# Kernel optimization log

Hardware: AMD Instinct MI355X
Metric: run time of the kernel (lower is better)

## Reference

```python
import jax, jax.numpy as jnp
import numpy as np

N_HEAD = 12
SEQ = 4096
D_MODEL = 768


def setup_inputs() -> dict:
    key = jax.random.key(0)
    ks = jax.random.split(key, 5)
    tokens = jax.random.normal(ks[0], (SEQ, D_MODEL), dtype=jnp.float32)
    # GPT-2 causal mask buffer: lower-triangular ones, shape [1,1,n_ctx,n_ctx]
    attn_bias = jnp.tril(jnp.ones((SEQ, SEQ), dtype=jnp.float32))[None, None]
    c_attn_weight = jax.random.normal(ks[1], (D_MODEL, 3 * D_MODEL), dtype=jnp.float32) * 0.02
    c_attn_bias = jax.random.normal(ks[2], (3 * D_MODEL,), dtype=jnp.float32) * 0.02
    c_proj_weight = jax.random.normal(ks[3], (D_MODEL, D_MODEL), dtype=jnp.float32) * 0.02
    c_proj_bias = jax.random.normal(ks[4], (D_MODEL,), dtype=jnp.float32) * 0.02
    return {
        "tokens": tokens,
        "attn_bias": attn_bias,
        "c_attn_weight": c_attn_weight,
        "c_attn_bias": c_attn_bias,
        "c_proj_weight": c_proj_weight,
        "c_proj_bias": c_proj_bias,
    }


def reference(tokens, attn_bias, c_attn_weight, c_attn_bias, c_proj_weight, c_proj_bias):
    S, D = tokens.shape
    H = N_HEAD
    hd = D // H
    qkv = tokens @ c_attn_weight + c_attn_bias          # [S, 3D]
    q, k, v = jnp.split(qkv, 3, axis=1)                 # each [S, D]
    q = q.reshape(S, H, hd).transpose(1, 0, 2)          # [H, S, hd]
    kh = k.reshape(S, H, hd).transpose(1, 2, 0)         # [H, hd, S] (key pre-transposed)
    vh = v.reshape(S, H, hd).transpose(1, 0, 2)         # [H, S, hd]
    w = jnp.einsum('hqd,hdk->hqk', q, kh) / jnp.sqrt(jnp.float32(hd))  # [H, S, S]
    nd, ns = S, S
    b = attn_bias[0, :, ns - nd:ns, :ns]                # [1, S, S], broadcasts over heads
    w = w * b - 1e10 * (1.0 - b)
    p = jax.nn.softmax(w, axis=-1)
    a = jnp.einsum('hqk,hkd->hqd', p, vh)               # [H, S, hd]
    a = a.transpose(1, 0, 2).reshape(S, D)              # merge heads
    out = a @ c_proj_weight + c_proj_bias               # [S, D]
    return out
```

## Files before the change

### kernel.cpp

```cpp
#include <hip/hip_runtime.h>

typedef __attribute__((ext_vector_type(8))) short s8v;
typedef __attribute__((ext_vector_type(4))) float f32x4;
typedef __attribute__((ext_vector_type(4))) unsigned short u16x4;
typedef __attribute__((ext_vector_type(2))) unsigned int u32x2;

#define SEQ 4096
#define DM  768
#define NH  12
#define HD  64

__device__ __forceinline__ unsigned short f2bf(float f) {
  union { float f; unsigned int u; } v; v.f = f;
  unsigned int r = v.u + 0x7fffu + ((v.u >> 16) & 1u);
  return (unsigned short)(r >> 16);
}

__device__ __forceinline__ unsigned int cvtpk(float lo, float hi) {
  unsigned int r;
  asm("v_cvt_pk_bf16_f32 %0, %1, %2" : "=v"(r) : "v"(lo), "v"(hi));
  return r;
}

__device__ __forceinline__ void gload16(const void* g, void* l) {
  __builtin_amdgcn_global_load_lds((const __attribute__((address_space(1))) void*)g,
                                   (__attribute__((address_space(3))) void*)l, 16, 0, 0);
}

__global__ __launch_bounds__(256) void k_cast(const float* __restrict__ in,
                                              unsigned short* __restrict__ out) {
  int i = (blockIdx.x * 256 + threadIdx.x) * 4;
  float4 v = *reinterpret_cast<const float4*>(in + i);
  u16x4 o;
  o.x = f2bf(v.x); o.y = f2bf(v.y); o.z = f2bf(v.z); o.w = f2bf(v.w);
  *reinterpret_cast<u16x4*>(out + i) = o;
}

__global__ __launch_bounds__(256) void k_transpose_cast(const float* __restrict__ in,
                                                        unsigned short* __restrict__ out,
                                                        int K, int N) {
  __shared__ float tile[32][33];
  int k0 = blockIdx.x * 32, n0 = blockIdx.y * 32;
  int tr = threadIdx.x >> 5, tc = threadIdx.x & 31;
#pragma unroll
  for (int i = 0; i < 4; i++)
    tile[i * 8 + tr][tc] = in[(k0 + i * 8 + tr) * N + n0 + tc];
  __syncthreads();
#pragma unroll
  for (int i = 0; i < 4; i++)
    out[(n0 + i * 8 + tr) * K + k0 + tc] = f2bf(tile[tc][i * 8 + tr]);
}

template<int MODE>
__global__ __launch_bounds__(256) void k_gemm(
    const unsigned short* __restrict__ A, const unsigned short* __restrict__ BT,
    const float* __restrict__ bias,
    unsigned short* __restrict__ Oq, unsigned short* __restrict__ Ok,
    unsigned short* __restrict__ Ov, float* __restrict__ Of) {
  __shared__ unsigned short As[128 * 32];
  __shared__ unsigned short Bs[128 * 32];
  const int tid = threadIdx.x;
  const int lane = tid & 63;
  const int w = tid >> 6;
  const int wm = w >> 1, wn = w & 1;
  const int l15 = lane & 15, l4 = lane >> 4;
  const int m0 = blockIdx.x * 128, n0 = blockIdx.y * 128;

  f32x4 acc[4][4] = {};

  int srow[2], skc[2];
#pragma unroll
  for (int j = 0; j < 2; j++) {
    int slot = j * 256 + tid;
    srow[j] = slot >> 2;
    skc[j] = (slot & 3) ^ ((srow[j] >> 1) & 3);
  }
  const int ldsb0 = (tid & ~63) * 16;
  const int ldsb1 = (256 + (tid & ~63)) * 16;

  for (int k0 = 0; k0 < DM; k0 += 32) {
    gload16(A + (m0 + srow[0]) * DM + k0 + skc[0] * 8, (char*)As + ldsb0);
    gload16(A + (m0 + srow[1]) * DM + k0 + skc[1] * 8, (char*)As + ldsb1);
    gload16(BT + (n0 + srow[0]) * DM + k0 + skc[0] * 8, (char*)Bs + ldsb0);
    gload16(BT + (n0 + srow[1]) * DM + k0 + skc[1] * 8, (char*)Bs + ldsb1);
    __syncthreads();
    s8v af[4], bfr[4];
#pragma unroll
    for (int i = 0; i < 4; i++) {
      int ra = wm * 64 + i * 16 + l15;
      int ca = (l4 ^ ((ra >> 1) & 3)) * 8;
      af[i] = *reinterpret_cast<const s8v*>(&As[ra * 32 + ca]);
      int rb = wn * 64 + i * 16 + l15;
      int cb = (l4 ^ ((rb >> 1) & 3)) * 8;
      bfr[i] = *reinterpret_cast<const s8v*>(&Bs[rb * 32 + cb]);
    }
#pragma unroll
    for (int mi = 0; mi < 4; mi++)
#pragma unroll
      for (int nj = 0; nj < 4; nj++)
        acc[mi][nj] = __builtin_amdgcn_mfma_f32_16x16x32_bf16(af[mi], bfr[nj], acc[mi][nj], 0, 0, 0);
    __syncthreads();
  }

#pragma unroll
  for (int nj = 0; nj < 4; nj++) {
    const int col = n0 + wn * 64 + nj * 16 + l15;
    const float bv = bias[col];
#pragma unroll
    for (int mi = 0; mi < 4; mi++) {
      const int rowb = m0 + wm * 64 + mi * 16 + l4 * 4;
      if (MODE == 0) {
        if (col < 768) {
#pragma unroll
          for (int r = 0; r < 4; r++)
            Oq[(rowb + r) * DM + col] = f2bf(acc[mi][nj][r] + bv);
        } else if (col < 1536) {
#pragma unroll
          for (int r = 0; r < 4; r++)
            Ok[(rowb + r) * DM + (col - 768)] = f2bf(acc[mi][nj][r] + bv);
        } else {
          u16x4 pk;
#pragma unroll
          for (int r = 0; r < 4; r++)
            pk[r] = f2bf(acc[mi][nj][r] + bv);
          *reinterpret_cast<u16x4*>(&Ov[(col - 1536) * SEQ + rowb]) = pk;
        }
      } else {
#pragma unroll
        for (int r = 0; r < 4; r++)
          Of[(rowb + r) * DM + col] = acc[mi][nj][r] + bv;
      }
    }
  }
}

__global__ __launch_bounds__(256, 4) void k_attn(
    const unsigned short* __restrict__ Qb, const unsigned short* __restrict__ Kb,
    const unsigned short* __restrict__ Vt, float* __restrict__ Opart,
    float* __restrict__ mlw) {
  __shared__ unsigned short Ks[2][64 * 64];
  __shared__ unsigned short Vs[2][64 * 64];
  __shared__ unsigned char Pl[4][2048];
  const int tid = threadIdx.x;
  const int lane = tid & 63;
  const int w = tid >> 6;
  const int l15 = lane & 15, l4 = lane >> 4;
  const int bid = blockIdx.x;
  const int s = bid & 1;
  const int b2 = bid >> 1;
  const int h = b2 % NH;
  const int qt = 63 - (b2 / NH);
  const int q0 = qt * 64 + w * 16;
  const int ntiles = qt + 1;
  const float SCL = 0.125f * 1.44269504f;

  const unsigned short* const Kh = Kb + h * HD;
  const unsigned short* const Vh = Vt + h * HD * SEQ;

  int srow[2], scol[2];
#pragma unroll
  for (int j = 0; j < 2; j++) {
    int c = j * 256 + tid;
    srow[j] = c >> 3;
    scol[j] = ((c & 7) ^ (srow[j] & 7)) * 8;
  }
  const int ldsoff0 = (tid & ~63) * 16;
  const int ldsoff1 = 4096 + (tid & ~63) * 16;

  s8v aq[2];
#pragma unroll
  for (int kc = 0; kc < 2; kc++)
    aq[kc] = *reinterpret_cast<const s8v*>(&Qb[(q0 + l15) * DM + h * HD + kc * 32 + l4 * 8]);

  const int kvbase = l15 * 128 + ((l4 ^ (l15 & 7)) << 4);

  unsigned char* const pw = (unsigned char*)&Pl[w][0];
  const int swz = (l15 & 7) << 4;
  const int wr_base = l15 * 128 + l4 * 8;
  const int rd_base = l15 * 128 + l4 * 16;
  const int lanediff = l15 - l4 * 4;

  f32x4 Ot[4] = {};
  float m = -1e30f, lsum = 0.f;

  if (s < ntiles) {
    const int kb0 = s * 64;
    gload16(Kh + (kb0 + srow[0]) * DM + scol[0], (char*)Ks[0] + ldsoff0);
    gload16(Kh + (kb0 + srow[1]) * DM + scol[1], (char*)Ks[0] + ldsoff1);
    gload16(Vh + srow[0] * SEQ + kb0 + scol[0], (char*)Vs[0] + ldsoff0);
    gload16(Vh + srow[1] * SEQ + kb0 + scol[1], (char*)Vs[0] + ldsoff1);
    __asm__ volatile("s_waitcnt vmcnt(0)" ::: "memory");
  }
  __syncthreads();

  for (int t = s; t < ntiles; t += 2) {
    const int cur = ((t - s) >> 1) & 1;
    if (t + 2 < ntiles) {
      const int kb2 = (t + 2) * 64;
      const int nxt = cur ^ 1;
      gload16(Kh + (kb2 + srow[0]) * DM + scol[0], (char*)Ks[nxt] + ldsoff0);
      gload16(Kh + (kb2 + srow[1]) * DM + scol[1], (char*)Ks[nxt] + ldsoff1);
      gload16(Vh + srow[0] * SEQ + kb2 + scol[0], (char*)Vs[nxt] + ldsoff0);
      gload16(Vh + srow[1] * SEQ + kb2 + scol[1], (char*)Vs[nxt] + ldsoff1);
    }
    const int kb = t * 64;
    const char* const kbuf = (const char*)Ks[cur];
    const char* const vbuf = (const char*)Vs[cur];

    float p[4][4];
#pragma unroll
    for (int c2 = 0; c2 < 4; c2++) {
      const s8v k0 = *reinterpret_cast<const s8v*>(kbuf + (c2 * 2048 + kvbase));
      const s8v k1 = *reinterpret_cast<const s8v*>(kbuf + ((c2 * 2048 + kvbase) ^ 64));
      f32x4 z = {};
      z = __builtin_amdgcn_mfma_f32_16x16x32_bf16(k0, aq[0], z, 0, 0, 0);
      z = __builtin_amdgcn_mfma_f32_16x16x32_bf16(k1, aq[1], z, 0, 0, 0);
#pragma unroll
      for (int r = 0; r < 4; r++) p[c2][r] = z[r];
    }
    if (kb + 63 > q0) {
      const int qml = q0 - kb + lanediff;
#pragma unroll
      for (int c2 = 0; c2 < 4; c2++)
#pragma unroll
        for (int r = 0; r < 4; r++)
          p[c2][r] = (c2 * 16 + r > qml) ? -1e30f : p[c2][r];
    }
    float t0 = fmaxf(fmaxf(p[0][0], p[0][1]), fmaxf(p[0][2], p[0][3]));
    float t1 = fmaxf(fmaxf(p[1][0], p[1][1]), fmaxf(p[1][2], p[1][3]));
    float t2 = fmaxf(fmaxf(p[2][0], p[2][1]), fmaxf(p[2][2], p[2][3]));
    float t3 = fmaxf(fmaxf(p[3][0], p[3][1]), fmaxf(p[3][2], p[3][3]));
    float tm = fmaxf(fmaxf(t0, t1), fmaxf(t2, t3));
    tm = fmaxf(tm, __shfl_xor(tm, 16));
    tm = fmaxf(tm, __shfl_xor(tm, 32));
    const float tsc = tm * SCL;
    if (!__all(tsc <= m + 8.f)) {
      const float mn = fmaxf(m, tsc);
      const float al = exp2f(m - mn);
      m = mn;
      lsum *= al;
#pragma unroll
      for (int dc = 0; dc < 4; dc++)
#pragma unroll
        for (int r = 0; r < 4; r++) Ot[dc][r] *= al;
    }
    float sacc = 0.f;
#pragma unroll
    for (int c2 = 0; c2 < 4; c2++) {
      float e0 = exp2f(fmaf(p[c2][0], SCL, -m));
      float e1 = exp2f(fmaf(p[c2][1], SCL, -m));
      float e2 = exp2f(fmaf(p[c2][2], SCL, -m));
      float e3 = exp2f(fmaf(p[c2][3], SCL, -m));
      sacc += (e0 + e1) + (e2 + e3);
      u32x2 pk;
      pk.x = cvtpk(e0, e1);
      pk.y = cvtpk(e2, e3);
      *reinterpret_cast<u32x2*>(pw + ((wr_base + c2 * 32) ^ swz)) = pk;
    }
    lsum += sacc;
    __asm__ volatile("s_waitcnt lgkmcnt(0)" ::: "memory");
    const s8v pb0 = *reinterpret_cast<const s8v*>(pw + (rd_base ^ swz));
    const s8v pb1 = *reinterpret_cast<const s8v*>(pw + ((rd_base + 64) ^ swz));
#pragma unroll
    for (int dc = 0; dc < 4; dc++) {
      const s8v v0 = *reinterpret_cast<const s8v*>(vbuf + (dc * 2048 + kvbase));
      const s8v v1 = *reinterpret_cast<const s8v*>(vbuf + ((dc * 2048 + kvbase) ^ 64));
      Ot[dc] = __builtin_amdgcn_mfma_f32_16x16x32_bf16(v0, pb0, Ot[dc], 0, 0, 0);
      Ot[dc] = __builtin_amdgcn_mfma_f32_16x16x32_bf16(v1, pb1, Ot[dc], 0, 0, 0);
    }
    __asm__ volatile("s_waitcnt vmcnt(0)" ::: "memory");
    __syncthreads();
  }

  lsum += __shfl_xor(lsum, 16);
  lsum += __shfl_xor(lsum, 32);
  float* const op = Opart + (size_t)s * SEQ * DM + (q0 + l15) * DM + h * HD;
#pragma unroll
  for (int dc = 0; dc < 4; dc++)
    *reinterpret_cast<f32x4*>(op + dc * 16 + l4 * 4) = Ot[dc];
  if (l4 == 0) {
    float2* const mp = (float2*)mlw;
    mp[(s * NH + h) * SEQ + q0 + l15] = make_float2(m, lsum);
  }
}

__global__ __launch_bounds__(256) void k_merge(const float* __restrict__ Opart,
                                               const float* __restrict__ mlw,
                                               unsigned short* __restrict__ attn) {
  const int idx = blockIdx.x * 256 + threadIdx.x;
  const int e4 = idx * 4;
  const int row = e4 / DM;
  const int col = e4 - row * DM;
  const int h = col >> 6;
  const float2* mp = (const float2*)mlw;
  const float2 a = mp[h * SEQ + row];
  const float2 b = mp[(NH + h) * SEQ + row];
  const float ms = fmaxf(a.x, b.x);
  const float w0 = exp2f(a.x - ms), w1 = exp2f(b.x - ms);
  const float rl = 1.f / (w0 * a.y + w1 * b.y);
  const float4 o0 = *reinterpret_cast<const float4*>(Opart + e4);
  const float4 o1 = *reinterpret_cast<const float4*>(Opart + (size_t)SEQ * DM + e4);
  u16x4 pk;
  pk.x = f2bf((w0 * o0.x + w1 * o1.x) * rl);
  pk.y = f2bf((w0 * o0.y + w1 * o1.y) * rl);
  pk.z = f2bf((w0 * o0.z + w1 * o1.z) * rl);
  pk.w = f2bf((w0 * o0.w + w1 * o1.w) * rl);
  *reinterpret_cast<u16x4*>(attn + e4) = pk;
}

extern "C" void kernel_launch(void* const* d_in, const int* in_sizes, int n_in,
                              void* d_out, int out_size, void* d_ws, size_t ws_size,
                              hipStream_t stream) {
  (void)in_sizes; (void)n_in; (void)out_size; (void)ws_size;
  const float* tokens = (const float*)d_in[0];
  const float* wqkv  = (const float*)d_in[2];
  const float* bqkv  = (const float*)d_in[3];
  const float* wproj = (const float*)d_in[4];
  const float* bproj = (const float*)d_in[5];
  float* out = (float*)d_out;

  unsigned short* tok    = (unsigned short*)d_ws;
  unsigned short* wqkvT  = tok + 4096 * 768;
  unsigned short* wprojT = wqkvT + 2304 * 768;
  unsigned short* Qb     = wprojT + 768 * 768;
  unsigned short* Kb     = Qb + 4096 * 768;
  unsigned short* Vt     = Kb + 4096 * 768;
  unsigned short* attn   = Vt + 768 * 4096;
  float* Opart = (float*)(attn + 4096 * 768);
  float* mlw   = Opart + 2 * 4096 * 768;

  k_cast<<<3072, 256, 0, stream>>>(tokens, tok);
  k_transpose_cast<<<dim3(24, 72), 256, 0, stream>>>(wqkv, wqkvT, 768, 2304);
  k_transpose_cast<<<dim3(24, 24), 256, 0, stream>>>(wproj, wprojT, 768, 768);
  k_gemm<0><<<dim3(32, 18), 256, 0, stream>>>(tok, wqkvT, bqkv, Qb, Kb, Vt, nullptr);
  k_attn<<<1536, 256, 0, stream>>>(Qb, Kb, Vt, Opart, mlw);
  k_merge<<<3072, 256, 0, stream>>>(Opart, mlw, attn);
  k_gemm<1><<<dim3(32, 6), 256, 0, stream>>>(attn, wprojT, bproj, nullptr, nullptr, nullptr, out);
}
```

Measured before the change: 119.1 us.

## Rework attention to 32x32 MFMA tiles with register-resident P and 4-way KV split

The attention kernel now uses 32x32x16 bf16 MFMAs with 128-query blocks (32 rows per wave). The softmax probabilities are repacked in registers via permlane32 swaps instead of going through an LDS round trip. The softmax scale and log2e are folded into Q inside the QKV GEMM epilogue. KV tiles are split across 4 blocks instead of 2, and the merge kernel combines four partials. This cuts LDS traffic and per-tile softmax instructions, but doubles the partial-output memory traffic in the merge and adds causal-skip imbalance.

New measurement: 138.1 us. 1.16x slower.

```diff
diff --git a/kernel.cpp b/kernel.cpp
--- a/kernel.cpp
+++ b/kernel.cpp
@@ -2,13 +2,15 @@
 
 typedef __attribute__((ext_vector_type(8))) short s8v;
 typedef __attribute__((ext_vector_type(4))) float f32x4;
+typedef __attribute__((ext_vector_type(16))) float f32x16;
 typedef __attribute__((ext_vector_type(4))) unsigned short u16x4;
-typedef __attribute__((ext_vector_type(2))) unsigned int u32x2;
+typedef __attribute__((ext_vector_type(4))) unsigned int u32x4;
 
 #define SEQ 4096
 #define DM  768
 #define NH  12
 #define HD  64
+#define QSCL 0.18033688f
 
 __device__ __forceinline__ unsigned short f2bf(float f) {
   union { float f; unsigned int u; } v; v.f = f;
@@ -113,7 +115,7 @@
         if (col < 768) {
 #pragma unroll
           for (int r = 0; r < 4; r++)
-            Oq[(rowb + r) * DM + col] = f2bf(acc[mi][nj][r] + bv);
+            Oq[(rowb + r) * DM + col] = f2bf((acc[mi][nj][r] + bv) * QSCL);
         } else if (col < 1536) {
 #pragma unroll
           for (int r = 0; r < 4; r++)
@@ -134,28 +136,26 @@
   }
 }
 
-__global__ __launch_bounds__(256, 4) void k_attn(
+__global__ __launch_bounds__(256, 5) void k_attn(
     const unsigned short* __restrict__ Qb, const unsigned short* __restrict__ Kb,
     const unsigned short* __restrict__ Vt, float* __restrict__ Opart,
     float* __restrict__ mlw) {
   __shared__ unsigned short Ks[2][64 * 64];
   __shared__ unsigned short Vs[2][64 * 64];
-  __shared__ unsigned char Pl[4][2048];
   const int tid = threadIdx.x;
   const int lane = tid & 63;
   const int w = tid >> 6;
-  const int l15 = lane & 15, l4 = lane >> 4;
+  const int l31 = lane & 31, lh = lane >> 5;
   const int bid = blockIdx.x;
-  const int s = bid & 1;
-  const int b2 = bid >> 1;
-  const int h = b2 % NH;
-  const int qt = 63 - (b2 / NH);
-  const int q0 = qt * 64 + w * 16;
-  const int ntiles = qt + 1;
-  const float SCL = 0.125f * 1.44269504f;
-
-  const unsigned short* const Kh = Kb + h * HD;
-  const unsigned short* const Vh = Vt + h * HD * SEQ;
+  const int s = bid & 3;
+  const int b2 = bid >> 2;
+  const int head = b2 % NH;
+  const int qt = 31 - (b2 / NH);
+  const int q0w = qt * 128 + w * 32;
+  const int ntiles = 2 * qt + 2;
+
+  const unsigned short* const Kh = Kb + head * HD;
+  const unsigned short* const Vh = Vt + head * HD * SEQ;
 
   int srow[2], scol[2];
 #pragma unroll
@@ -167,20 +167,16 @@
   const int ldsoff0 = (tid & ~63) * 16;
   const int ldsoff1 = 4096 + (tid & ~63) * 16;
 
-  s8v aq[2];
-#pragma unroll
-  for (int kc = 0; kc < 2; kc++)
-    aq[kc] = *reinterpret_cast<const s8v*>(&Qb[(q0 + l15) * DM + h * HD + kc * 32 + l4 * 8]);
-
-  const int kvbase = l15 * 128 + ((l4 ^ (l15 & 7)) << 4);
-
-  unsigned char* const pw = (unsigned char*)&Pl[w][0];
-  const int swz = (l15 & 7) << 4;
-  const int wr_base = l15 * 128 + l4 * 8;
-  const int rd_base = l15 * 128 + l4 * 16;
-  const int lanediff = l15 - l4 * 4;
-
-  f32x4 Ot[4] = {};
+  s8v aq[4];
+#pragma unroll
+  for (int kc = 0; kc < 4; kc++)
+    aq[kc] = *reinterpret_cast<const s8v*>(
+        &Qb[(q0w + l31) * DM + head * HD + kc * 16 + lh * 8]);
+
+  const int x7 = l31 & 7;
+  const int rbase = l31 * 128;
+
+  f32x16 O0 = {}, O1 = {};
   float m = -1e30f, lsum = 0.f;
 
   if (s < ntiles) {
@@ -193,10 +189,10 @@
   }
   __syncthreads();
 
-  for (int t = s; t < ntiles; t += 2) {
-    const int cur = ((t - s) >> 1) & 1;
-    if (t + 2 < ntiles) {
-      const int kb2 = (t + 2) * 64;
+  for (int t = s; t < ntiles; t += 4) {
+    const int cur = ((t - s) >> 2) & 1;
+    if (t + 4 < ntiles) {
+      const int kb2 = (t + 4) * 64;
       const int nxt = cur ^ 1;
       gload16(Kh + (kb2 + srow[0]) * DM + scol[0], (char*)Ks[nxt] + ldsoff0);
       gload16(Kh + (kb2 + srow[1]) * DM + scol[1], (char*)Ks[nxt] + ldsoff1);
@@ -204,83 +200,94 @@
       gload16(Vh + srow[1] * SEQ + kb2 + scol[1], (char*)Vs[nxt] + ldsoff1);
     }
     const int kb = t * 64;
-    const char* const kbuf = (const char*)Ks[cur];
-    const char* const vbuf = (const char*)Vs[cur];
-
-    float p[4][4];
-#pragma unroll
-    for (int c2 = 0; c2 < 4; c2++) {
-      const s8v k0 = *reinterpret_cast<const s8v*>(kbuf + (c2 * 2048 + kvbase));
-      const s8v k1 = *reinterpret_cast<const s8v*>(kbuf + ((c2 * 2048 + kvbase) ^ 64));
-      f32x4 z = {};
-      z = __builtin_amdgcn_mfma_f32_16x16x32_bf16(k0, aq[0], z, 0, 0, 0);
-      z = __builtin_amdgcn_mfma_f32_16x16x32_bf16(k1, aq[1], z, 0, 0, 0);
-#pragma unroll
-      for (int r = 0; r < 4; r++) p[c2][r] = z[r];
-    }
-    if (kb + 63 > q0) {
-      const int qml = q0 - kb + lanediff;
-#pragma unroll
-      for (int c2 = 0; c2 < 4; c2++)
-#pragma unroll
-        for (int r = 0; r < 4; r++)
-          p[c2][r] = (c2 * 16 + r > qml) ? -1e30f : p[c2][r];
-    }
-    float t0 = fmaxf(fmaxf(p[0][0], p[0][1]), fmaxf(p[0][2], p[0][3]));
-    float t1 = fmaxf(fmaxf(p[1][0], p[1][1]), fmaxf(p[1][2], p[1][3]));
-    float t2 = fmaxf(fmaxf(p[2][0], p[2][1]), fmaxf(p[2][2], p[2][3]));
-    float t3 = fmaxf(fmaxf(p[3][0], p[3][1]), fmaxf(p[3][2], p[3][3]));
-    float tm = fmaxf(fmaxf(t0, t1), fmaxf(t2, t3));
-    tm = fmaxf(tm, __shfl_xor(tm, 16));
-    tm = fmaxf(tm, __shfl_xor(tm, 32));
-    const float tsc = tm * SCL;
-    if (!__all(tsc <= m + 8.f)) {
-      const float mn = fmaxf(m, tsc);
-      const float al = exp2f(m - mn);
-      m = mn;
-      lsum *= al;
-#pragma unroll
-      for (int dc = 0; dc < 4; dc++)
-#pragma unroll
-        for (int r = 0; r < 4; r++) Ot[dc][r] *= al;
-    }
-    float sacc = 0.f;
-#pragma unroll
-    for (int c2 = 0; c2 < 4; c2++) {
-      float e0 = exp2f(fmaf(p[c2][0], SCL, -m));
-      float e1 = exp2f(fmaf(p[c2][1], SCL, -m));
-      float e2 = exp2f(fmaf(p[c2][2], SCL, -m));
-      float e3 = exp2f(fmaf(p[c2][3], SCL, -m));
-      sacc += (e0 + e1) + (e2 + e3);
-      u32x2 pk;
-      pk.x = cvtpk(e0, e1);
-      pk.y = cvtpk(e2, e3);
-      *reinterpret_cast<u32x2*>(pw + ((wr_base + c2 * 32) ^ swz)) = pk;
-    }
-    lsum += sacc;
-    __asm__ volatile("s_waitcnt lgkmcnt(0)" ::: "memory");
-    const s8v pb0 = *reinterpret_cast<const s8v*>(pw + (rd_base ^ swz));
-    const s8v pb1 = *reinterpret_cast<const s8v*>(pw + ((rd_base + 64) ^ swz));
-#pragma unroll
-    for (int dc = 0; dc < 4; dc++) {
-      const s8v v0 = *reinterpret_cast<const s8v*>(vbuf + (dc * 2048 + kvbase));
-      const s8v v1 = *reinterpret_cast<const s8v*>(vbuf + ((dc * 2048 + kvbase) ^ 64));
-      Ot[dc] = __builtin_amdgcn_mfma_f32_16x16x32_bf16(v0, pb0, Ot[dc], 0, 0, 0);
-      Ot[dc] = __builtin_amdgcn_mfma_f32_16x16x32_bf16(v1, pb1, Ot[dc], 0, 0, 0);
+    if (kb <= q0w + 31) {
+      const char* const kbuf = (const char*)Ks[cur];
+      const char* const vbuf = (const char*)Vs[cur];
+      f32x16 z0 = {}, z1 = {};
+#pragma unroll
+      for (int kc = 0; kc < 4; kc++) {
+        const int so = ((kc * 2 + lh) ^ x7) << 4;
+        const s8v k0 = *reinterpret_cast<const s8v*>(kbuf + rbase + so);
+        const s8v k1 = *reinterpret_cast<const s8v*>(kbuf + 4096 + rbase + so);
+        z0 = __builtin_amdgcn_mfma_f32_32x32x16_bf16(k0, aq[kc], z0, 0, 0, 0);
+        z1 = __builtin_amdgcn_mfma_f32_32x32x16_bf16(k1, aq[kc], z1, 0, 0, 0);
+      }
+      float p0[16], p1[16];
+#pragma unroll
+      for (int r = 0; r < 16; r++) { p0[r] = z0[r]; p1[r] = z1[r]; }
+      if (kb + 63 > q0w) {
+        const int qm = q0w + l31 - kb - 4 * lh;
+#pragma unroll
+        for (int r = 0; r < 16; r++) {
+          const int koff = (r & 3) + 8 * (r >> 2);
+          p0[r] = (koff > qm) ? -1e30f : p0[r];
+          p1[r] = (koff + 32 > qm) ? -1e30f : p1[r];
+        }
+      }
+      float tm = p0[0];
+#pragma unroll
+      for (int r = 1; r < 16; r++) tm = fmaxf(tm, p0[r]);
+#pragma unroll
+      for (int r = 0; r < 16; r++) tm = fmaxf(tm, p1[r]);
+      tm = fmaxf(tm, __shfl_xor(tm, 32));
+      if (!__all(tm <= m + 8.f)) {
+        const float mn = fmaxf(m, tm);
+        const float al = exp2f(m - mn);
+        m = mn;
+        lsum *= al;
+#pragma unroll
+        for (int r = 0; r < 16; r++) { O0[r] *= al; O1[r] *= al; }
+      }
+      float sacc = 0.f;
+#pragma unroll
+      for (int r = 0; r < 16; r++) { p0[r] = exp2f(p0[r] - m); sacc += p0[r]; }
+#pragma unroll
+      for (int r = 0; r < 16; r++) { p1[r] = exp2f(p1[r] - m); sacc += p1[r]; }
+      lsum += sacc;
+      s8v pf[4];
+#define PACKKC(pp, dst)                                                      \
+      {                                                                      \
+        unsigned int A0 = cvtpk(pp[0], pp[1]);                               \
+        unsigned int B0 = cvtpk(pp[2], pp[3]);                               \
+        unsigned int A1 = cvtpk(pp[4], pp[5]);                               \
+        unsigned int B1 = cvtpk(pp[6], pp[7]);                               \
+        asm("v_permlane32_swap_b32 %0, %1" : "+v"(A0), "+v"(A1));            \
+        asm("v_permlane32_swap_b32 %0, %1" : "+v"(B0), "+v"(B1));            \
+        u32x4 q_ = {A0, B0, A1, B1};                                         \
+        dst = __builtin_bit_cast(s8v, q_);                                   \
+      }
+      PACKKC(p0, pf[0]);
+      PACKKC((p0 + 8), pf[1]);
+      PACKKC(p1, pf[2]);
+      PACKKC((p1 + 8), pf[3]);
+#undef PACKKC
+#pragma unroll
+      for (int kc = 0; kc < 4; kc++) {
+        const int so = ((kc * 2 + lh) ^ x7) << 4;
+        const s8v v0 = *reinterpret_cast<const s8v*>(vbuf + rbase + so);
+        const s8v v1 = *reinterpret_cast<const s8v*>(vbuf + 4096 + rbase + so);
+        O0 = __builtin_amdgcn_mfma_f32_32x32x16_bf16(v0, pf[kc], O0, 0, 0, 0);
+        O1 = __builtin_amdgcn_mfma_f32_32x32x16_bf16(v1, pf[kc], O1, 0, 0, 0);
+      }
     }
     __asm__ volatile("s_waitcnt vmcnt(0)" ::: "memory");
     __syncthreads();
   }
 
-  lsum += __shfl_xor(lsum, 16);
   lsum += __shfl_xor(lsum, 32);
-  float* const op = Opart + (size_t)s * SEQ * DM + (q0 + l15) * DM + h * HD;
-#pragma unroll
-  for (int dc = 0; dc < 4; dc++)
-    *reinterpret_cast<f32x4*>(op + dc * 16 + l4 * 4) = Ot[dc];
-  if (l4 == 0) {
+  float* const op = Opart + (size_t)s * SEQ * DM + (size_t)(q0w + l31) * DM +
+                    head * HD + 4 * lh;
+#pragma unroll
+  for (int k = 0; k < 4; k++) {
+    f32x4 o0, o1;
+#pragma unroll
+    for (int r = 0; r < 4; r++) { o0[r] = O0[k * 4 + r]; o1[r] = O1[k * 4 + r]; }
+    *reinterpret_cast<f32x4*>(op + 8 * k) = o0;
+    *reinterpret_cast<f32x4*>(op + 32 + 8 * k) = o1;
+  }
+  if (lh == 0) {
     float2* const mp = (float2*)mlw;
-    mp[(s * NH + h) * SEQ + q0 + l15] = make_float2(m, lsum);
+    mp[(s * NH + head) * SEQ + q0w + l31] = make_float2(m, lsum);
   }
 }
 
@@ -291,20 +298,26 @@
   const int e4 = idx * 4;
   const int row = e4 / DM;
   const int col = e4 - row * DM;
-  const int h = col >> 6;
+  const int head = col >> 6;
   const float2* mp = (const float2*)mlw;
-  const float2 a = mp[h * SEQ + row];
-  const float2 b = mp[(NH + h) * SEQ + row];
-  const float ms = fmaxf(a.x, b.x);
-  const float w0 = exp2f(a.x - ms), w1 = exp2f(b.x - ms);
-  const float rl = 1.f / (w0 * a.y + w1 * b.y);
+  const float2 a0 = mp[(0 * NH + head) * SEQ + row];
+  const float2 a1 = mp[(1 * NH + head) * SEQ + row];
+  const float2 a2 = mp[(2 * NH + head) * SEQ + row];
+  const float2 a3 = mp[(3 * NH + head) * SEQ + row];
+  const float ms = fmaxf(fmaxf(a0.x, a1.x), fmaxf(a2.x, a3.x));
+  const float w0 = exp2f(a0.x - ms), w1 = exp2f(a1.x - ms);
+  const float w2 = exp2f(a2.x - ms), w3 = exp2f(a3.x - ms);
+  const float rl = 1.f / (w0 * a0.y + w1 * a1.y + w2 * a2.y + w3 * a3.y);
+  const size_t SD = (size_t)SEQ * DM;
   const float4 o0 = *reinterpret_cast<const float4*>(Opart + e4);
-  const float4 o1 = *reinterpret_cast<const float4*>(Opart + (size_t)SEQ * DM + e4);
+  const float4 o1 = *reinterpret_cast<const float4*>(Opart + SD + e4);
+  const float4 o2 = *reinterpret_cast<const float4*>(Opart + 2 * SD + e4);
+  const float4 o3 = *reinterpret_cast<const float4*>(Opart + 3 * SD + e4);
   u16x4 pk;
-  pk.x = f2bf((w0 * o0.x + w1 * o1.x) * rl);
-  pk.y = f2bf((w0 * o0.y + w1 * o1.y) * rl);
-  pk.z = f2bf((w0 * o0.z + w1 * o1.z) * rl);
-  pk.w = f2bf((w0 * o0.w + w1 * o1.w) * rl);
+  pk.x = f2bf((w0 * o0.x + w1 * o1.x + w2 * o2.x + w3 * o3.x) * rl);
+  pk.y = f2bf((w0 * o0.y + w1 * o1.y + w2 * o2.y + w3 * o3.y) * rl);
+  pk.z = f2bf((w0 * o0.z + w1 * o1.z + w2 * o2.z + w3 * o3.z) * rl);
+  pk.w = f2bf((w0 * o0.w + w1 * o1.w + w2 * o2.w + w3 * o3.w) * rl);
   *reinterpret_cast<u16x4*>(attn + e4) = pk;
 }
 
@@ -327,7 +340,7 @@
   unsigned short* Vt     = Kb + 4096 * 768;
   unsigned short* attn   = Vt + 768 * 4096;
   float* Opart = (float*)(attn + 4096 * 768);
-  float* mlw   = Opart + 2 * 4096 * 768;
+  float* mlw   = Opart + 4 * 4096 * 768;
 
   k_cast<<<3072, 256, 0, stream>>>(tokens, tok);
   k_transpose_cast<<<dim3(24, 72), 256, 0, stream>>>(wqkv, wqkvT, 768, 2304);
```
